# Performance work log

Hardware: AMD Instinct MI355X
Metric: run time of the kernel (lower is better)

The kernel has to match this reference:

```python
import jax, jax.numpy as jnp
import numpy as np

N = 20000      # nodes
E = 320000     # edges (avg degree 16)
IN = 128
HID = 64
CLS = 32
H0, H1, H2 = 4, 4, 6
SLOPE = 0.2


def _lin(key, fan_in, fan_out):
    kw, kb = jax.random.split(key)
    s = 1.0 / np.sqrt(fan_in)
    W = jax.random.uniform(kw, (fan_in, fan_out), minval=-s, maxval=s, dtype=jnp.float32)
    b = jax.random.uniform(kb, (fan_out,), minval=-s, maxval=s, dtype=jnp.float32)
    return W, b


def setup_inputs() -> dict:
    key = jax.random.key(0)
    ks = jax.random.split(key, 16)
    x = jax.random.normal(ks[0], (N, IN), dtype=jnp.float32)
    src = jax.random.randint(ks[1], (E,), 0, N)
    dst = jax.random.randint(ks[2], (E,), 0, N)
    W0s, b0s = _lin(ks[3], IN, H0 * HID)
    W0d, b0d = _lin(ks[4], IN, H0 * HID)
    a0 = jax.random.normal(ks[5], (H0, HID), dtype=jnp.float32) * 0.05
    d1 = H0 * HID  # 256, flattened hidden width
    W1s, b1s = _lin(ks[6], d1, H1 * HID)
    W1d, b1d = _lin(ks[7], d1, H1 * HID)
    a1 = jax.random.normal(ks[8], (H1, HID), dtype=jnp.float32) * 0.05
    W2s, b2s = _lin(ks[9], d1, H2 * CLS)
    W2d, b2d = _lin(ks[10], d1, H2 * CLS)
    a2 = jax.random.normal(ks[11], (H2, CLS), dtype=jnp.float32) * 0.05
    Wr2, br2 = _lin(ks[12], d1, H2 * CLS)  # residual projection (256 != 192)
    return dict(x=x, src=src, dst=dst,
                W0s=W0s, b0s=b0s, W0d=W0d, b0d=b0d, a0=a0,
                W1s=W1s, b1s=b1s, W1d=W1d, b1d=b1d, a1=a1,
                W2s=W2s, b2s=b2s, W2d=W2d, b2d=b2d, a2=a2,
                Wr2=Wr2, br2=br2)


def _gatv2_layer(x, src, dst, Ws, bs, Wd, bd, attn, heads, dim, res, act):
    n = x.shape[0]
    feat_src = (x @ Ws + bs).reshape(n, heads, dim)
    feat_dst = (x @ Wd + bd).reshape(n, heads, dim)
    # GATv2 edge scores: a^T LeakyReLU(W_l h_u + W_r h_v)
    e = jax.nn.leaky_relu(feat_src[src] + feat_dst[dst], SLOPE)  # [E,H,D]
    logits = jnp.einsum('ehd,hd->eh', e, attn)                    # [E,H]
    # numerically-stable edge softmax over incoming edges per destination
    m = jax.ops.segment_max(logits, dst, num_segments=n)
    m = jnp.where(jnp.isfinite(m), m, 0.0)
    ex = jnp.exp(logits - m[dst])
    denom = jax.ops.segment_sum(ex, dst, num_segments=n)
    alpha = ex / denom[dst]                                        # [E,H]
    out = jax.ops.segment_sum(feat_src[src] * alpha[:, :, None], dst, num_segments=n)
    if res == 'id':
        out = out + x.reshape(n, heads, dim)
    elif res is not None:
        Wr, br = res
        out = out + (x @ Wr + br).reshape(n, heads, dim)
    if act:
        out = jax.nn.elu(out)
    return out  # [n, heads, dim]


def reference(x, src, dst,
              W0s, b0s, W0d, b0d, a0,
              W1s, b1s, W1d, b1d, a1,
              W2s, b2s, W2d, b2d, a2,
              Wr2, br2):
    h = _gatv2_layer(x, src, dst, W0s, b0s, W0d, b0d, a0, H0, HID, None, True)
    h = h.reshape(N, H0 * HID)
    h = _gatv2_layer(h, src, dst, W1s, b1s, W1d, b1d, a1, H1, HID, 'id', True)
    h = h.reshape(N, H1 * HID)
    out = _gatv2_layer(h, src, dst, W2s, b2s, W2d, b2d, a2, H2, CLS, (Wr2, br2), False)
    return out.mean(axis=1)  # [N, num_classes]
```

## Files before the change

kernel.cpp:

```cpp
#include <hip/hip_runtime.h>
#include <hip/hip_bf16.h>
#include <float.h>
#include <math.h>

#define NN 20000
#define EE 320000
#define IN_DIM 128
#define DEG_CAP 64

typedef __attribute__((ext_vector_type(4))) float f32x4;
typedef _Float16 f16;
typedef __attribute__((ext_vector_type(2))) _Float16 f16x2;
typedef __attribute__((ext_vector_type(4))) _Float16 f16x4;
typedef __attribute__((ext_vector_type(8))) _Float16 f16x8;

typedef const unsigned int __attribute__((address_space(1)))* gas_u32p;
typedef unsigned int __attribute__((address_space(3)))* las_u32p;

#define LOG2E 1.4426950408889634f

template <int CTRL>
__device__ __forceinline__ float dpp_add(float v) {
    int x = __builtin_amdgcn_update_dpp(0, __builtin_bit_cast(int, v), CTRL, 0xF, 0xF, false);
    return v + __builtin_bit_cast(float, x);
}
template <int GSZ>
__device__ __forceinline__ float group_sum(float v) {
    if constexpr (GSZ == 8) v = dpp_add<0x141>(v);
    v = dpp_add<0xB1>(v);
    v = dpp_add<0x4E>(v);
    return v;
}

__device__ __forceinline__ void prep_elem(const float* __restrict__ Wa, const float* __restrict__ ba, int na,
                                          const float* __restrict__ Wb, const float* __restrict__ bb, int nb,
                                          const float* __restrict__ Wc, const float* __restrict__ bc, int nc,
                                          int K, f16* __restrict__ Wt, float* __restrict__ bias_cat, int idx) {
    int n = idx / K;
    int k = idx - n * K;
    const float* W; const float* b; int nl; int ncols;
    if (n < na) { W = Wa; b = ba; nl = n; ncols = na; }
    else if (n < na + nb) { W = Wb; b = bb; nl = n - na; ncols = nb; }
    else { W = Wc; b = bc; nl = n - na - nb; ncols = nc; }
    Wt[(size_t)n * K + k] = (f16)W[(size_t)k * ncols + nl];
    if (k == 0) bias_cat[n] = b[nl];
}

#define SEG0 (512 * 128)
#define SEG1 (512 * 256)
#define SEG2 (576 * 256)
#define SEG3 (NN * IN_DIM / 4)
__global__ void prep_all(const float* __restrict__ W0s, const float* __restrict__ b0s,
                         const float* __restrict__ W0d, const float* __restrict__ b0d,
                         const float* __restrict__ W1s, const float* __restrict__ b1s,
                         const float* __restrict__ W1d, const float* __restrict__ b1d,
                         const float* __restrict__ W2s, const float* __restrict__ b2s,
                         const float* __restrict__ W2d, const float* __restrict__ b2d,
                         const float* __restrict__ Wr2, const float* __restrict__ br2,
                         const float* __restrict__ x,
                         f16* __restrict__ Wt0, float* __restrict__ bias0,
                         f16* __restrict__ Wt1, float* __restrict__ bias1,
                         f16* __restrict__ Wt2, float* __restrict__ bias2,
                         f16* __restrict__ A) {
    int idx = blockIdx.x * 256 + threadIdx.x;
    if (idx < SEG0) {
        prep_elem(W0s, b0s, 256, W0d, b0d, 256, nullptr, nullptr, 0, 128, Wt0, bias0, idx);
    } else if ((idx -= SEG0) < SEG1) {
        prep_elem(W1s, b1s, 256, W1d, b1d, 256, nullptr, nullptr, 0, 256, Wt1, bias1, idx);
    } else if ((idx -= SEG1) < SEG2) {
        prep_elem(W2s, b2s, 192, W2d, b2d, 192, Wr2, br2, 192, 256, Wt2, bias2, idx);
    } else if ((idx -= SEG2) < SEG3) {
        float4 v = ((const float4*)x)[idx];
        f16x4 o = {(f16)v.x, (f16)v.y, (f16)v.z, (f16)v.w};
        ((f16x4*)A)[idx] = o;
    }
}

template <int K>
__global__ __launch_bounds__(256) void gemm_mfma_f16(
        const f16* __restrict__ A, const f16* __restrict__ Wt,
        const float* __restrict__ bias,
        f16* __restrict__ F0, f16* __restrict__ F1, float* __restrict__ F2,
        int b1, int b2, int M, int S, int gx, int gy,
        int SB, const int* __restrict__ esrc, const int* __restrict__ edst,
        unsigned int* __restrict__ cursor, int* __restrict__ csr_dst, int E) {
    constexpr int K32 = K / 32;
    constexpr int BSN = (64 * K > 4 * 32 * 66) ? 64 * K : 4 * 32 * 66;
    __shared__ f16 Bs[BSN];

    if (blockIdx.x < (unsigned)SB) {
        int e = blockIdx.x * 256 + threadIdx.x;
        if (e < E) {
            int d = edst[e];
            unsigned pos = atomicAdd(&cursor[d], 1u);
            if (pos < DEG_CAP) csr_dst[(unsigned)d * DEG_CAP + pos] = esrc[e];
        }
        return;
    }
    const int bid = blockIdx.x - SB;

    const int p = bid & 7;
    const int q = bid >> 3;
    const int bn_i = q % gx;
    const int bm_i = (q / gx) * 8 + p;
    if (bm_i >= gy) return;
    const int bm = bm_i * 128;
    const int bn = bn_i * 64;

    const int tid = threadIdx.x;
    const int wave = tid >> 6;
    const int lane = tid & 63;
    const int m16 = lane & 15;
    const int quad = lane >> 4;

    {
        const f16* gs = Wt + (size_t)(bn + 16 * wave + m16) * K + quad * 8;
        #pragma unroll
        for (int j = 0; j < K32; ++j) {
            __builtin_amdgcn_global_load_lds(
                (gas_u32p)(const void*)(gs + j * 32),
                (las_u32p)(void*)(&Bs[((j * 4 + wave) * 64) * 8]),
                16, 0, 0);
        }
    }

    const int rb0 = bm + wave * 32;
    int ar[2];
    #pragma unroll
    for (int mt = 0; mt < 2; ++mt) {
        int row = rb0 + mt * 16 + m16;
        ar[mt] = row < M ? row : M - 1;
    }

    f16x8 ahr[2][K32];
    #pragma unroll
    for (int mt = 0; mt < 2; ++mt) {
        const f16* ap = A + (size_t)ar[mt] * K + quad * 8;
        #pragma unroll
        for (int kc = 0; kc < K32; ++kc)
            ahr[mt][kc] = *(const f16x8*)(ap + kc * 32);
    }

    __syncthreads();

    f32x4 acc[2][4];
    #pragma unroll
    for (int mt = 0; mt < 2; ++mt)
        #pragma unroll
        for (int nt = 0; nt < 4; ++nt) acc[mt][nt] = (f32x4){0.f, 0.f, 0.f, 0.f};

    #pragma unroll
    for (int kc = 0; kc < K32; ++kc) {
        f16x8 bs[4];
        #pragma unroll
        for (int nt = 0; nt < 4; ++nt)
            bs[nt] = *(const f16x8*)&Bs[((kc * 4 + nt) * 64 + lane) * 8];
        #pragma unroll
        for (int nt = 0; nt < 4; ++nt)
            #pragma unroll
            for (int mt = 0; mt < 2; ++mt)
                acc[mt][nt] = __builtin_amdgcn_mfma_f32_16x16x32_f16(ahr[mt][kc], bs[nt], acc[mt][nt], 0, 0, 0);
    }

    __syncthreads();
    f16* Cs = Bs;

    if (bn < b2) {
        f16* __restrict__ Fb;
        int cs, cb;
        if (bn >= b1) { Fb = F1; cb = bn - b1; cs = b2 - b1; }
        else          { Fb = F0; cb = bn;      cs = b1; }
        f16* cw = Cs + wave * (32 * 66);
        #pragma unroll
        for (int nt = 0; nt < 4; ++nt) {
            float bv = bias[bn + nt * 16 + m16];
            #pragma unroll
            for (int mt = 0; mt < 2; ++mt)
                #pragma unroll
                for (int r = 0; r < 4; ++r) {
                    int row = mt * 16 + quad * 4 + r;
                    cw[row * 66 + nt * 16 + m16] = (f16)(acc[mt][nt][r] + bv);
                }
        }
        int lrow = lane >> 1;
        int lcol = (lane & 1) * 32;
        int grow = rb0 + lrow;
        if (grow < M) {
            #pragma unroll
            for (int j = 0; j < 4; ++j) {
                f16x8 v = *(f16x8*)&cw[lrow * 66 + lcol + j * 8];
                *(f16x8*)&Fb[(size_t)grow * cs + cb + lcol + j * 8] = v;
            }
        }
    } else {
        int cs = S - b2;
        #pragma unroll
        for (int nt = 0; nt < 4; ++nt) {
            int col = bn - b2 + nt * 16 + m16;
            float bv = bias[bn + nt * 16 + m16];
            #pragma unroll
            for (int mt = 0; mt < 2; ++mt)
                #pragma unroll
                for (int r = 0; r < 4; ++r) {
                    int row = rb0 + mt * 16 + quad * 4 + r;
                    if (row < M) F2[(size_t)row * cs + col] = acc[mt][nt][r] + bv;
                }
        }
    }
}

#define AGG_STEP(U0, CNT)                                                     \
    _Pragma("unroll")                                                         \
    for (int uu = 0; uu < (CNT); ++uu) {                                      \
        const int u = (U0) + uu;                                              \
        const f16x8 cur = buf[u];                                             \
        const unsigned su = (unsigned)cidx[u];                                \
        buf[u] = *(const f16x8*)&fsb[su * (unsigned)HD + off];                \
        cidx[u] = csr_l[nib64 + b + 16 + u];                                  \
        float pp = 0.f;                                                       \
        _Pragma("unroll")                                                     \
        for (int i = 0; i < 4; ++i) {                                         \
            f16x2 cp = (f16x2){cur[2 * i], cur[2 * i + 1]};                   \
            f16x2 xp = cp + fdp[i];                                           \
            unsigned xu = __builtin_bit_cast(unsigned, xp) & 0x7FFF7FFFu;     \
            f16x2 xa = __builtin_bit_cast(f16x2, xu);                         \
            pp = __builtin_amdgcn_fdot2(xp, a6p[i], pp, false);               \
            pp = __builtin_amdgcn_fdot2(xa, a4p[i], pp, false);               \
        }                                                                     \
        pp = group_sum<GSZ>(pp);                                              \
        float w = (b + u < dg) ? __builtin_amdgcn_exp2f(pp) : 0.f;            \
        lh += w;                                                              \
        _Pragma("unroll")                                                     \
        for (int d = 0; d < 8; ++d) acc[d] += w * (float)cur[d];              \
    }

template <int HD, int D, bool HAS_RES, bool DO_ELU, int OUT_MODE>
__global__ __launch_bounds__(256) void gat_node_aggregate(
        const f16* __restrict__ fsb, const f16* __restrict__ fdb,
        const float* __restrict__ attn,
        const unsigned int* __restrict__ degv,
        const int* __restrict__ csr_src,
        const float* __restrict__ resid, int RS,
        float* __restrict__ outF, f16* __restrict__ outA) {
    constexpr int LANES = HD / 8;
    constexpr int GSZ = D / 8;
    __shared__ int csr_l[544];
    __shared__ float red[(OUT_MODE == 2) ? 8 : 1][(OUT_MODE == 2) ? HD : 1];

    {
        int i = threadIdx.x;
        csr_l[i]       = csr_src[(size_t)blockIdx.x * 512 + i];
        csr_l[i + 256] = csr_src[(size_t)blockIdx.x * 512 + i + 256];
        if (i < 32) csr_l[512 + i] = 0;
    }

    const int wave = threadIdx.x >> 6;
    const int lane = threadIdx.x & 63;
    const int half = lane >> 5;
    const int ln = lane & 31;
    const int t = blockIdx.x * 8 + wave * 2 + half;
    const bool active = (ln < LANES);
    const unsigned off = active ? 8u * ln : 0u;
    const int nib64 = (wave * 2 + half) * 64;

    f16x2 fdp[4], a6p[4], a4p[4];
    if (active) {
        f16x8 dv = *(const f16x8*)&fdb[(unsigned)t * HD + off];
        float4 aA = *(const float4*)&attn[off];
        float4 aB = *(const float4*)&attn[off + 4];
        float av[8] = {aA.x, aA.y, aA.z, aA.w, aB.x, aB.y, aB.z, aB.w};
        #pragma unroll
        for (int i = 0; i < 4; ++i) {
            fdp[i] = (f16x2){dv[2 * i], dv[2 * i + 1]};
            a6p[i] = (f16x2){(f16)(0.6f * LOG2E * av[2 * i]), (f16)(0.6f * LOG2E * av[2 * i + 1])};
            a4p[i] = (f16x2){(f16)(0.4f * LOG2E * av[2 * i]), (f16)(0.4f * LOG2E * av[2 * i + 1])};
        }
    } else {
        #pragma unroll
        for (int i = 0; i < 4; ++i) {
            fdp[i] = (f16x2){0, 0}; a6p[i] = (f16x2){0, 0}; a4p[i] = (f16x2){0, 0};
        }
    }

    const int dg = min((int)degv[t], DEG_CAP);
    const int degO = __shfl_xor(dg, 32, 64);
    const int mdeg = max(dg, degO);

    float acc[8];
    #pragma unroll
    for (int d = 0; d < 8; ++d) acc[d] = 0.f;
    float lh = 0.f;

    __syncthreads();

    f16x8 buf[8];
    int cidx[8];
    #pragma unroll
    for (int u = 0; u < 8; ++u) {
        unsigned s0 = (unsigned)csr_l[nib64 + u];
        buf[u] = *(const f16x8*)&fsb[s0 * (unsigned)HD + off];
        cidx[u] = csr_l[nib64 + 8 + u];
    }

    int b = 0;
    for (; b + 8 <= mdeg; b += 8) {
        AGG_STEP(0, 4)
        AGG_STEP(4, 4)
    }
    {
        const int rem = mdeg - b;
        if (rem > 0) { AGG_STEP(0, 2) }
        if (rem > 2) { AGG_STEP(2, 2) }
        if (rem > 4) { AGG_STEP(4, 2) }
        if (rem > 6) { AGG_STEP(6, 2) }
    }

    float inv = (lh > 0.f) ? 1.f / lh : 0.f;
    float vout[8];
    #pragma unroll
    for (int d = 0; d < 8; ++d) vout[d] = acc[d] * inv;
    if (HAS_RES && active) {
        float4 rA = *(const float4*)&resid[(unsigned)t * RS + off];
        float4 rB = *(const float4*)&resid[(unsigned)t * RS + off + 4];
        vout[0] += rA.x; vout[1] += rA.y; vout[2] += rA.z; vout[3] += rA.w;
        vout[4] += rB.x; vout[5] += rB.y; vout[6] += rB.z; vout[7] += rB.w;
    }
    if (DO_ELU) {
        #pragma unroll
        for (int d = 0; d < 8; ++d) vout[d] = vout[d] > 0.f ? vout[d] : expm1f(vout[d]);
    }

    if (OUT_MODE == 2) {
        const int nib = wave * 2 + half;
        if (active) {
            *(float4*)&red[nib][off] = make_float4(vout[0], vout[1], vout[2], vout[3]);
            *(float4*)&red[nib][off + 4] = make_float4(vout[4], vout[5], vout[6], vout[7]);
        }
        __syncthreads();
        int node = threadIdx.x >> 5;
        int col = threadIdx.x & 31;
        float ssum = 0.f;
        #pragma unroll
        for (int h = 0; h < 6; ++h) ssum += red[node][h * 32 + col];
        outF[(unsigned)(blockIdx.x * 8 + node) * 32 + col] = ssum * (1.f / 6.f);
    } else if (active) {
        f16x8 av;
        #pragma unroll
        for (int d = 0; d < 8; ++d) av[d] = (f16)vout[d];
        *(f16x8*)&outA[(unsigned)t * HD + off] = av;
        if (OUT_MODE == 0) {
            *(float4*)&outF[(unsigned)t * HD + off] = make_float4(vout[0], vout[1], vout[2], vout[3]);
            *(float4*)&outF[(unsigned)t * HD + off + 4] = make_float4(vout[4], vout[5], vout[6], vout[7]);
        }
    }
}

extern "C" void kernel_launch(void* const* d_in, const int* in_sizes, int n_in,
                              void* d_out, int out_size, void* d_ws, size_t ws_size,
                              hipStream_t stream) {
    const float* x   = (const float*)d_in[0];
    const int*   src = (const int*)d_in[1];
    const int*   dst = (const int*)d_in[2];
    const float* W0s = (const float*)d_in[3];
    const float* b0s = (const float*)d_in[4];
    const float* W0d = (const float*)d_in[5];
    const float* b0d = (const float*)d_in[6];
    const float* a0  = (const float*)d_in[7];
    const float* W1s = (const float*)d_in[8];
    const float* b1s = (const float*)d_in[9];
    const float* W1d = (const float*)d_in[10];
    const float* b1d = (const float*)d_in[11];
    const float* a1  = (const float*)d_in[12];
    const float* W2s = (const float*)d_in[13];
    const float* b2s = (const float*)d_in[14];
    const float* W2d = (const float*)d_in[15];
    const float* b2d = (const float*)d_in[16];
    const float* a2  = (const float*)d_in[17];
    const float* Wr2 = (const float*)d_in[18];
    const float* br2 = (const float*)d_in[19];

    f16* FsH = (f16*)d_ws;
    f16* FdH = FsH + (size_t)NN * 256;
    f16* A   = FdH + (size_t)NN * 256;
    float* O0 = (float*)(A + (size_t)NN * 256);
    f16* Wt0 = (f16*)(O0 + (size_t)NN * 256);
    f16* Wt1 = Wt0 + 512 * 128;
    f16* Wt2 = Wt1 + 512 * 256;
    float* bias0 = (float*)(Wt2 + 576 * 256);
    float* bias1 = bias0 + 512;
    float* bias2 = bias1 + 512;
    unsigned int* deg = (unsigned int*)(bias2 + 576);
    int* csr_src      = (int*)(deg + NN);

    hipMemsetAsync(deg, 0, (size_t)NN * 4 + (size_t)NN * DEG_CAP * 4, stream);
    {
        int total = SEG0 + SEG1 + SEG2 + SEG3;
        prep_all<<<(total + 255) / 256, 256, 0, stream>>>(
            W0s, b0s, W0d, b0d, W1s, b1s, W1d, b1d, W2s, b2s, W2d, b2d, Wr2, br2, x,
            Wt0, bias0, Wt1, bias1, Wt2, bias2, A);
    }

    const int gy = (NN + 127) / 128;
    const int gy8 = ((gy + 7) / 8) * 8;
    const int nagg = NN / 8;
    const int sblk = (EE + 255) / 256;

    gemm_mfma_f16<128><<<sblk + gy8 * 8, 256, 0, stream>>>(A, Wt0, bias0,
                                               FsH, FdH, nullptr, 256, 512, NN, 512, 8, gy,
                                               sblk, src, dst, deg, csr_src, EE);
    gat_node_aggregate<256, 64, false, true, 0><<<nagg, 256, 0, stream>>>(
        FsH, FdH, a0, deg, csr_src, nullptr, 0, O0, A);

    gemm_mfma_f16<256><<<gy8 * 8, 256, 0, stream>>>(A, Wt1, bias1,
                                               FsH, FdH, nullptr, 256, 512, NN, 512, 8, gy,
                                               0, nullptr, nullptr, nullptr, nullptr, 0);
    gat_node_aggregate<256, 64, true, true, 1><<<nagg, 256, 0, stream>>>(
        FsH, FdH, a1, deg, csr_src, O0, 256, nullptr, A);

    gemm_mfma_f16<256><<<gy8 * 9, 256, 0, stream>>>(A, Wt2, bias2,
                                               FsH, FdH, O0, 192, 384, NN, 576, 9, gy,
                                               0, nullptr, nullptr, nullptr, nullptr, 0);
    gat_node_aggregate<192, 32, true, false, 2><<<nagg, 256, 0, stream>>>(
        FsH, FdH, a2, deg, csr_src, O0, 192, (float*)d_out, nullptr);
}
```

Before: 269.2 us.

## Fuse weight transpose/convert and input cast into GEMM kernels, drop prep kernel

Removes the separate prep kernel that transposed the fp32 weights to f16 and cast x to f16. Each GEMM block now reads its fp32 weight slice directly, converts it, and writes it into LDS. The first-layer GEMM also loads fp32 x and converts it in registers. This saves one launch and an intermediate round trip, but every block now redoes the weight conversion with strided scalar loads instead of async global-to-LDS copies.

```diff
diff --git a/kernel.cpp b/kernel.cpp
--- a/kernel.cpp
+++ b/kernel.cpp
@@ -13,9 +13,6 @@
 typedef __attribute__((ext_vector_type(2))) _Float16 f16x2;
 typedef __attribute__((ext_vector_type(4))) _Float16 f16x4;
 typedef __attribute__((ext_vector_type(8))) _Float16 f16x8;
-
-typedef const unsigned int __attribute__((address_space(1)))* gas_u32p;
-typedef unsigned int __attribute__((address_space(3)))* las_u32p;
 
 #define LOG2E 1.4426950408889634f
 
@@ -32,54 +29,12 @@
     return v;
 }
 
-__device__ __forceinline__ void prep_elem(const float* __restrict__ Wa, const float* __restrict__ ba, int na,
-                                          const float* __restrict__ Wb, const float* __restrict__ bb, int nb,
-                                          const float* __restrict__ Wc, const float* __restrict__ bc, int nc,
-                                          int K, f16* __restrict__ Wt, float* __restrict__ bias_cat, int idx) {
-    int n = idx / K;
-    int k = idx - n * K;
-    const float* W; const float* b; int nl; int ncols;
-    if (n < na) { W = Wa; b = ba; nl = n; ncols = na; }
-    else if (n < na + nb) { W = Wb; b = bb; nl = n - na; ncols = nb; }
-    else { W = Wc; b = bc; nl = n - na - nb; ncols = nc; }
-    Wt[(size_t)n * K + k] = (f16)W[(size_t)k * ncols + nl];
-    if (k == 0) bias_cat[n] = b[nl];
-}
-
-#define SEG0 (512 * 128)
-#define SEG1 (512 * 256)
-#define SEG2 (576 * 256)
-#define SEG3 (NN * IN_DIM / 4)
-__global__ void prep_all(const float* __restrict__ W0s, const float* __restrict__ b0s,
-                         const float* __restrict__ W0d, const float* __restrict__ b0d,
-                         const float* __restrict__ W1s, const float* __restrict__ b1s,
-                         const float* __restrict__ W1d, const float* __restrict__ b1d,
-                         const float* __restrict__ W2s, const float* __restrict__ b2s,
-                         const float* __restrict__ W2d, const float* __restrict__ b2d,
-                         const float* __restrict__ Wr2, const float* __restrict__ br2,
-                         const float* __restrict__ x,
-                         f16* __restrict__ Wt0, float* __restrict__ bias0,
-                         f16* __restrict__ Wt1, float* __restrict__ bias1,
-                         f16* __restrict__ Wt2, float* __restrict__ bias2,
-                         f16* __restrict__ A) {
-    int idx = blockIdx.x * 256 + threadIdx.x;
-    if (idx < SEG0) {
-        prep_elem(W0s, b0s, 256, W0d, b0d, 256, nullptr, nullptr, 0, 128, Wt0, bias0, idx);
-    } else if ((idx -= SEG0) < SEG1) {
-        prep_elem(W1s, b1s, 256, W1d, b1d, 256, nullptr, nullptr, 0, 256, Wt1, bias1, idx);
-    } else if ((idx -= SEG1) < SEG2) {
-        prep_elem(W2s, b2s, 192, W2d, b2d, 192, Wr2, br2, 192, 256, Wt2, bias2, idx);
-    } else if ((idx -= SEG2) < SEG3) {
-        float4 v = ((const float4*)x)[idx];
-        f16x4 o = {(f16)v.x, (f16)v.y, (f16)v.z, (f16)v.w};
-        ((f16x4*)A)[idx] = o;
-    }
-}
-
-template <int K>
-__global__ __launch_bounds__(256) void gemm_mfma_f16(
-        const f16* __restrict__ A, const f16* __restrict__ Wt,
-        const float* __restrict__ bias,
+template <int K, bool AF32>
+__global__ __launch_bounds__(256) void gemm_fused(
+        const void* __restrict__ Av,
+        const float* __restrict__ Wa, const float* __restrict__ ba, int na,
+        const float* __restrict__ Wb, const float* __restrict__ bb, int nb,
+        const float* __restrict__ Wc, const float* __restrict__ bc,
         f16* __restrict__ F0, f16* __restrict__ F1, float* __restrict__ F2,
         int b1, int b2, int M, int S, int gx, int gy,
         int SB, const int* __restrict__ esrc, const int* __restrict__ edst,
@@ -113,14 +68,24 @@
     const int m16 = lane & 15;
     const int quad = lane >> 4;
 
+    const float* Wsrc; const float* bsrc; int ncols, cbl;
+    if (bn < na)           { Wsrc = Wa; bsrc = ba; ncols = na;           cbl = bn; }
+    else if (bn < na + nb) { Wsrc = Wb; bsrc = bb; ncols = nb;           cbl = bn - na; }
+    else                   { Wsrc = Wc; bsrc = bc; ncols = S - na - nb;  cbl = bn - na - nb; }
+
     {
-        const f16* gs = Wt + (size_t)(bn + 16 * wave + m16) * K + quad * 8;
-        #pragma unroll
-        for (int j = 0; j < K32; ++j) {
-            __builtin_amdgcn_global_load_lds(
-                (gas_u32p)(const void*)(gs + j * 32),
-                (las_u32p)(void*)(&Bs[((j * 4 + wave) * 64) * 8]),
-                16, 0, 0);
+        #pragma unroll
+        for (int pass = 0; pass < K32; ++pass) {
+            const int k0 = pass * 32 + wave * 8;
+            const float* wp = Wsrc + (size_t)k0 * ncols + cbl + lane;
+            float v[8];
+            #pragma unroll
+            for (int j = 0; j < 8; ++j) v[j] = wp[(size_t)j * ncols];
+            f16x8 h;
+            #pragma unroll
+            for (int j = 0; j < 8; ++j) h[j] = (f16)v[j];
+            int chunk = (pass * 4 + (lane >> 4)) * 64 + wave * 16 + (lane & 15);
+            *(f16x8*)&Bs[chunk * 8] = h;
         }
     }
 
@@ -135,10 +100,21 @@
     f16x8 ahr[2][K32];
     #pragma unroll
     for (int mt = 0; mt < 2; ++mt) {
-        const f16* ap = A + (size_t)ar[mt] * K + quad * 8;
-        #pragma unroll
-        for (int kc = 0; kc < K32; ++kc)
-            ahr[mt][kc] = *(const f16x8*)(ap + kc * 32);
+        if constexpr (AF32) {
+            const float* ap = (const float*)Av + (size_t)ar[mt] * K + quad * 8;
+            #pragma unroll
+            for (int kc = 0; kc < K32; ++kc) {
+                float4 u = *(const float4*)(ap + kc * 32);
+                float4 w = *(const float4*)(ap + kc * 32 + 4);
+                ahr[mt][kc] = (f16x8){(f16)u.x, (f16)u.y, (f16)u.z, (f16)u.w,
+                                      (f16)w.x, (f16)w.y, (f16)w.z, (f16)w.w};
+            }
+        } else {
+            const f16* ap = (const f16*)Av + (size_t)ar[mt] * K + quad * 8;
+            #pragma unroll
+            for (int kc = 0; kc < K32; ++kc)
+                ahr[mt][kc] = *(const f16x8*)(ap + kc * 32);
+        }
     }
 
     __syncthreads();
@@ -173,7 +149,7 @@
         f16* cw = Cs + wave * (32 * 66);
         #pragma unroll
         for (int nt = 0; nt < 4; ++nt) {
-            float bv = bias[bn + nt * 16 + m16];
+            float bv = bsrc[cbl + nt * 16 + m16];
             #pragma unroll
             for (int mt = 0; mt < 2; ++mt)
                 #pragma unroll
@@ -197,7 +173,7 @@
         #pragma unroll
         for (int nt = 0; nt < 4; ++nt) {
             int col = bn - b2 + nt * 16 + m16;
-            float bv = bias[bn + nt * 16 + m16];
+            float bv = bsrc[cbl + nt * 16 + m16];
             #pragma unroll
             for (int mt = 0; mt < 2; ++mt)
                 #pragma unroll
@@ -383,43 +359,34 @@
     f16* FdH = FsH + (size_t)NN * 256;
     f16* A   = FdH + (size_t)NN * 256;
     float* O0 = (float*)(A + (size_t)NN * 256);
-    f16* Wt0 = (f16*)(O0 + (size_t)NN * 256);
-    f16* Wt1 = Wt0 + 512 * 128;
-    f16* Wt2 = Wt1 + 512 * 256;
-    float* bias0 = (float*)(Wt2 + 576 * 256);
-    float* bias1 = bias0 + 512;
-    float* bias2 = bias1 + 512;
-    unsigned int* deg = (unsigned int*)(bias2 + 576);
+    unsigned int* deg = (unsigned int*)(O0 + (size_t)NN * 256);
     int* csr_src      = (int*)(deg + NN);
 
     hipMemsetAsync(deg, 0, (size_t)NN * 4 + (size_t)NN * DEG_CAP * 4, stream);
-    {
-        int total = SEG0 + SEG1 + SEG2 + SEG3;
-        prep_all<<<(total + 255) / 256, 256, 0, stream>>>(
-            W0s, b0s, W0d, b0d, W1s, b1s, W1d, b1d, W2s, b2s, W2d, b2d, Wr2, br2, x,
-            Wt0, bias0, Wt1, bias1, Wt2, bias2, A);
-    }
 
     const int gy = (NN + 127) / 128;
     const int gy8 = ((gy + 7) / 8) * 8;
     const int nagg = NN / 8;
     const int sblk = (EE + 255) / 256;
 
-    gemm_mfma_f16<128><<<sblk + gy8 * 8, 256, 0, stream>>>(A, Wt0, bias0,
-                                               FsH, FdH, nullptr, 256, 512, NN, 512, 8, gy,
-                                               sblk, src, dst, deg, csr_src, EE);
+    gemm_fused<128, true><<<sblk + gy8 * 8, 256, 0, stream>>>(
+        x, W0s, b0s, 256, W0d, b0d, 256, nullptr, nullptr,
+        FsH, FdH, nullptr, 256, 512, NN, 512, 8, gy,
+        sblk, src, dst, deg, csr_src, EE);
     gat_node_aggregate<256, 64, false, true, 0><<<nagg, 256, 0, stream>>>(
         FsH, FdH, a0, deg, csr_src, nullptr, 0, O0, A);
 
-    gemm_mfma_f16<256><<<gy8 * 8, 256, 0, stream>>>(A, Wt1, bias1,
-                                               FsH, FdH, nullptr, 256, 512, NN, 512, 8, gy,
-                                               0, nullptr, nullptr, nullptr, nullptr, 0);
+    gemm_fused<256, false><<<gy8 * 8, 256, 0, stream>>>(
+        A, W1s, b1s, 256, W1d, b1d, 256, nullptr, nullptr,
+        FsH, FdH, nullptr, 256, 512, NN, 512, 8, gy,
+        0, nullptr, nullptr, nullptr, nullptr, 0);
     gat_node_aggregate<256, 64, true, true, 1><<<nagg, 256, 0, stream>>>(
         FsH, FdH, a1, deg, csr_src, O0, 256, nullptr, A);
 
-    gemm_mfma_f16<256><<<gy8 * 9, 256, 0, stream>>>(A, Wt2, bias2,
-                                               FsH, FdH, O0, 192, 384, NN, 576, 9, gy,
-                                               0, nullptr, nullptr, nullptr, nullptr, 0);
+    gemm_fused<256, false><<<gy8 * 9, 256, 0, stream>>>(
+        A, W2s, b2s, 192, W2d, b2d, 192, Wr2, br2,
+        FsH, FdH, O0, 192, 384, NN, 576, 9, gy,
+        0, nullptr, nullptr, nullptr, nullptr, 0);
     gat_node_aggregate<192, 32, true, false, 2><<<nagg, 256, 0, stream>>>(
         FsH, FdH, a2, deg, csr_src, O0, 192, (float*)d_out, nullptr);
 }
```

After: 253.2 us (median of 2 runs). -5.9%, faster.

## Loop over column tiles per block to reuse A rows in registers

Applied to the files above, without the earlier changes.

Each GEMM block now keeps its 128-row A tile in registers and loops over half of the output column tiles, loading a new W tile into shared memory each iteration. The grid shrinks from gy8*gx blocks to gy8*2. A separate shared buffer for the epilogue is added. This removes redundant global reads of A across column blocks, at the cost of fewer blocks (about 320), serialized W loads with two barriers per tile, and more shared memory per block.

```diff
diff --git a/kernel.cpp b/kernel.cpp
--- a/kernel.cpp
+++ b/kernel.cpp
@@ -85,8 +85,8 @@
         int SB, const int* __restrict__ esrc, const int* __restrict__ edst,
         unsigned int* __restrict__ cursor, int* __restrict__ csr_dst, int E) {
     constexpr int K32 = K / 32;
-    constexpr int BSN = (64 * K > 4 * 32 * 66) ? 64 * K : 4 * 32 * 66;
-    __shared__ f16 Bs[BSN];
+    __shared__ f16 Bs[64 * K];
+    __shared__ f16 Cs[4][32 * 66];
 
     if (blockIdx.x < (unsigned)SB) {
         int e = blockIdx.x * 256 + threadIdx.x;
@@ -101,28 +101,19 @@
 
     const int p = bid & 7;
     const int q = bid >> 3;
-    const int bn_i = q % gx;
-    const int bm_i = (q / gx) * 8 + p;
+    const int cg = q & 1;
+    const int bm_i = (q >> 1) * 8 + p;
     if (bm_i >= gy) return;
     const int bm = bm_i * 128;
-    const int bn = bn_i * 64;
+    const int chalf = (gx + 1) >> 1;
+    const int c0 = cg * chalf;
+    const int cnt = cg ? (gx - chalf) : chalf;
 
     const int tid = threadIdx.x;
     const int wave = tid >> 6;
     const int lane = tid & 63;
     const int m16 = lane & 15;
     const int quad = lane >> 4;
-
-    {
-        const f16* gs = Wt + (size_t)(bn + 16 * wave + m16) * K + quad * 8;
-        #pragma unroll
-        for (int j = 0; j < K32; ++j) {
-            __builtin_amdgcn_global_load_lds(
-                (gas_u32p)(const void*)(gs + j * 32),
-                (las_u32p)(void*)(&Bs[((j * 4 + wave) * 64) * 8]),
-                16, 0, 0);
-        }
-    }
 
     const int rb0 = bm + wave * 32;
     int ar[2];
@@ -141,70 +132,82 @@
             ahr[mt][kc] = *(const f16x8*)(ap + kc * 32);
     }
 
-    __syncthreads();
-
-    f32x4 acc[2][4];
-    #pragma unroll
-    for (int mt = 0; mt < 2; ++mt)
-        #pragma unroll
-        for (int nt = 0; nt < 4; ++nt) acc[mt][nt] = (f32x4){0.f, 0.f, 0.f, 0.f};
-
-    #pragma unroll
-    for (int kc = 0; kc < K32; ++kc) {
-        f16x8 bs[4];
-        #pragma unroll
-        for (int nt = 0; nt < 4; ++nt)
-            bs[nt] = *(const f16x8*)&Bs[((kc * 4 + nt) * 64 + lane) * 8];
-        #pragma unroll
-        for (int nt = 0; nt < 4; ++nt)
-            #pragma unroll
-            for (int mt = 0; mt < 2; ++mt)
-                acc[mt][nt] = __builtin_amdgcn_mfma_f32_16x16x32_f16(ahr[mt][kc], bs[nt], acc[mt][nt], 0, 0, 0);
-    }
-
-    __syncthreads();
-    f16* Cs = Bs;
-
-    if (bn < b2) {
-        f16* __restrict__ Fb;
-        int cs, cb;
-        if (bn >= b1) { Fb = F1; cb = bn - b1; cs = b2 - b1; }
-        else          { Fb = F0; cb = bn;      cs = b1; }
-        f16* cw = Cs + wave * (32 * 66);
-        #pragma unroll
-        for (int nt = 0; nt < 4; ++nt) {
-            float bv = bias[bn + nt * 16 + m16];
-            #pragma unroll
-            for (int mt = 0; mt < 2; ++mt)
+    for (int j = 0; j < cnt; ++j) {
+        const int bn = (c0 + j) * 64;
+        __syncthreads();
+
+        {
+            const f16* gs = Wt + (size_t)(bn + 16 * wave + m16) * K + quad * 8;
+            #pragma unroll
+            for (int kk = 0; kk < K32; ++kk) {
+                __builtin_amdgcn_global_load_lds(
+                    (gas_u32p)(const void*)(gs + kk * 32),
+                    (las_u32p)(void*)(&Bs[((kk * 4 + wave) * 64) * 8]),
+                    16, 0, 0);
+            }
+        }
+        __syncthreads();
+
+        f32x4 acc[2][4];
+        #pragma unroll
+        for (int mt = 0; mt < 2; ++mt)
+            #pragma unroll
+            for (int nt = 0; nt < 4; ++nt) acc[mt][nt] = (f32x4){0.f, 0.f, 0.f, 0.f};
+
+        #pragma unroll
+        for (int kc = 0; kc < K32; ++kc) {
+            f16x8 bs[4];
+            #pragma unroll
+            for (int nt = 0; nt < 4; ++nt)
+                bs[nt] = *(const f16x8*)&Bs[((kc * 4 + nt) * 64 + lane) * 8];
+            #pragma unroll
+            for (int nt = 0; nt < 4; ++nt)
                 #pragma unroll
-                for (int r = 0; r < 4; ++r) {
-                    int row = mt * 16 + quad * 4 + r;
-                    cw[row * 66 + nt * 16 + m16] = (f16)(acc[mt][nt][r] + bv);
+                for (int mt = 0; mt < 2; ++mt)
+                    acc[mt][nt] = __builtin_amdgcn_mfma_f32_16x16x32_f16(ahr[mt][kc], bs[nt], acc[mt][nt], 0, 0, 0);
+        }
+
+        if (bn < b2) {
+            f16* __restrict__ Fb;
+            int cs, cb;
+            if (bn >= b1) { Fb = F1; cb = bn - b1; cs = b2 - b1; }
+            else          { Fb = F0; cb = bn;      cs = b1; }
+            f16* cw = &Cs[wave][0];
+            #pragma unroll
+            for (int nt = 0; nt < 4; ++nt) {
+                float bv = bias[bn + nt * 16 + m16];
+                #pragma unroll
+                for (int mt = 0; mt < 2; ++mt)
+                    #pragma unroll
+                    for (int r = 0; r < 4; ++r) {
+                        int row = mt * 16 + quad * 4 + r;
+                        cw[row * 66 + nt * 16 + m16] = (f16)(acc[mt][nt][r] + bv);
+                    }
+            }
+            int lrow = lane >> 1;
+            int lcol = (lane & 1) * 32;
+            int grow = rb0 + lrow;
+            if (grow < M) {
+                #pragma unroll
+                for (int jj = 0; jj < 4; ++jj) {
+                    f16x8 v = *(f16x8*)&cw[lrow * 66 + lcol + jj * 8];
+                    *(f16x8*)&Fb[(size_t)grow * cs + cb + lcol + jj * 8] = v;
                 }
-        }
-        int lrow = lane >> 1;
-        int lcol = (lane & 1) * 32;
-        int grow = rb0 + lrow;
-        if (grow < M) {
-            #pragma unroll
-            for (int j = 0; j < 4; ++j) {
-                f16x8 v = *(f16x8*)&cw[lrow * 66 + lcol + j * 8];
-                *(f16x8*)&Fb[(size_t)grow * cs + cb + lcol + j * 8] = v;
             }
-        }
-    } else {
-        int cs = S - b2;
-        #pragma unroll
-        for (int nt = 0; nt < 4; ++nt) {
-            int col = bn - b2 + nt * 16 + m16;
-            float bv = bias[bn + nt * 16 + m16];
-            #pragma unroll
-            for (int mt = 0; mt < 2; ++mt)
+        } else {
+            int cs = S - b2;
+            #pragma unroll
+            for (int nt = 0; nt < 4; ++nt) {
+                int col = bn - b2 + nt * 16 + m16;
+                float bv = bias[bn + nt * 16 + m16];
                 #pragma unroll
-                for (int r = 0; r < 4; ++r) {
-                    int row = rb0 + mt * 16 + quad * 4 + r;
-                    if (row < M) F2[(size_t)row * cs + col] = acc[mt][nt][r] + bv;
-                }
+                for (int mt = 0; mt < 2; ++mt)
+                    #pragma unroll
+                    for (int r = 0; r < 4; ++r) {
+                        int row = rb0 + mt * 16 + quad * 4 + r;
+                        if (row < M) F2[(size_t)row * cs + col] = acc[mt][nt][r] + bv;
+                    }
+            }
         }
     }
 }
@@ -393,6 +396,7 @@
     int* csr_src      = (int*)(deg + NN);
 
     hipMemsetAsync(deg, 0, (size_t)NN * 4 + (size_t)NN * DEG_CAP * 4, stream);
+
     {
         int total = SEG0 + SEG1 + SEG2 + SEG3;
         prep_all<<<(total + 255) / 256, 256, 0, stream>>>(
@@ -404,20 +408,21 @@
     const int gy8 = ((gy + 7) / 8) * 8;
     const int nagg = NN / 8;
     const int sblk = (EE + 255) / 256;
-
-    gemm_mfma_f16<128><<<sblk + gy8 * 8, 256, 0, stream>>>(A, Wt0, bias0,
+    const int gg = gy8 * 2;
+
+    gemm_mfma_f16<128><<<sblk + gg, 256, 0, stream>>>(A, Wt0, bias0,
                                                FsH, FdH, nullptr, 256, 512, NN, 512, 8, gy,
                                                sblk, src, dst, deg, csr_src, EE);
     gat_node_aggregate<256, 64, false, true, 0><<<nagg, 256, 0, stream>>>(
         FsH, FdH, a0, deg, csr_src, nullptr, 0, O0, A);
 
-    gemm_mfma_f16<256><<<gy8 * 8, 256, 0, stream>>>(A, Wt1, bias1,
+    gemm_mfma_f16<256><<<gg, 256, 0, stream>>>(A, Wt1, bias1,
                                                FsH, FdH, nullptr, 256, 512, NN, 512, 8, gy,
                                                0, nullptr, nullptr, nullptr, nullptr, 0);
     gat_node_aggregate<256, 64, true, true, 1><<<nagg, 256, 0, stream>>>(
         FsH, FdH, a1, deg, csr_src, O0, 256, nullptr, A);
 
-    gemm_mfma_f16<256><<<gy8 * 9, 256, 0, stream>>>(A, Wt2, bias2,
+    gemm_mfma_f16<256><<<gg, 256, 0, stream>>>(A, Wt2, bias2,
                                                FsH, FdH, O0, 192, 384, NN, 576, 9, gy,
                                                0, nullptr, nullptr, nullptr, nullptr, 0);
     gat_node_aggregate<192, 32, true, false, 2><<<nagg, 256, 0, stream>>>(
```

New measurement: 275.1 us. +2.2%, slower.
